# Performance work log

Hardware: AMD Instinct MI355X
Metric: run time of the kernel (lower is better)

Reference implementation:

```python
import jax, jax.numpy as jnp
import numpy as np

N = 100000
E = 3200000
C = 32

def setup_inputs() -> dict:
    key = jax.random.key(0)
    k1, k2, k3, k4 = jax.random.split(key, 4)
    adj = jax.random.uniform(k1, (E,), dtype=jnp.float32)          # per-edge weights
    labels = jax.random.uniform(k2, (N, C), dtype=jnp.float32)     # node label distributions
    src = jax.random.randint(k3, (E,), 0, N, dtype=jnp.int64)
    dst = jax.random.randint(k4, (E,), 0, N, dtype=jnp.int64)
    return {"adj": adj, "labels": labels, "src": src, "dst": dst, "n_lpa": 3}

def reference(adj, labels, src, dst, n_lpa):
    # One hop of label propagation: msg_e = label[src_e] * w_e; out_v = sum_{e: dst_e=v} msg_e
    n_nodes = labels.shape[0]

    def lp(lab):
        msg = lab[src] * adj[:, None]                 # [E, C] gather-multiply
        return jax.ops.segment_sum(msg, dst, num_segments=n_nodes)  # scatter-sum over dst

    # soft_label == 0 path of the original forward: plain iterated propagation
    for _ in range(n_lpa):
        labels = lp(labels)
    return labels
```

## Files before the change

### kernel.cpp

```cpp
#include <hip/hip_runtime.h>
#include <hip/hip_bf16.h>


#define LPA_C   32
#define BKT_LG  7
#define BKT_NV  (1 << BKT_LG)
#define CHUNK   12800

__global__ __launch_bounds__(1024)
void k_histA(const int* __restrict__ dst, int* __restrict__ C,
             int E, int P, int nbkt) {
    __shared__ int h[1024];
    int c = blockIdx.x;
    int base = c * CHUNK;
    int lim = min(CHUNK, E - base);
    for (int i = threadIdx.x; i < nbkt; i += 1024) h[i] = 0;
    __syncthreads();
    for (int i = threadIdx.x; i < lim; i += 1024)
        atomicAdd(&h[dst[base + i] >> BKT_LG], 1);
    __syncthreads();
    for (int i = threadIdx.x; i < nbkt; i += 1024) C[i * P + c] = h[i];
}

__global__ void k_scanC(int* __restrict__ C, int* __restrict__ btot, int P) {
    __shared__ int s[256];
    int b = blockIdx.x;
    int t = threadIdx.x;
    int v = (t < P) ? C[b * P + t] : 0;
    s[t] = v;
    __syncthreads();
    for (int off = 1; off < 256; off <<= 1) {
        int x = (t >= off) ? s[t - off] : 0;
        __syncthreads();
        s[t] += x;
        __syncthreads();
    }
    if (t < P) C[b * P + t] = s[t] - v;
    if (t == 255) btot[b] = s[255];
}

__global__ __launch_bounds__(1024)
void k_scanB(const int* __restrict__ btot, int* __restrict__ bstart,
             int* __restrict__ row_start, int nb, int N, int E) {
    __shared__ int s[1024];
    int t = threadIdx.x;
    int v = (t < nb) ? btot[t] : 0;
    s[t] = v;
    __syncthreads();
    for (int off = 1; off < 1024; off <<= 1) {
        int x = (t >= off) ? s[t - off] : 0;
        __syncthreads();
        s[t] += x;
        __syncthreads();
    }
    if (t < nb) bstart[t] = s[t] - v;
    if (t == 0) { bstart[nb] = E; row_start[N] = E; }
}

__global__ __launch_bounds__(1024)
void k_scatA(const int* __restrict__ src, const int* __restrict__ dst,
             const float* __restrict__ adj, const int* __restrict__ C,
             const int* __restrict__ bstart, int2* __restrict__ mid,
             int E, int P, int nbkt) {
    __shared__ int cur[1024];
    int c = blockIdx.x;
    int base = c * CHUNK;
    int lim = min(CHUNK, E - base);
    for (int i = threadIdx.x; i < nbkt; i += 1024)
        cur[i] = bstart[i] + C[i * P + c];
    __syncthreads();
    for (int i = threadIdx.x; i < lim; i += 1024) {
        int d = dst[base + i];
        int b = d >> BKT_LG;
        int pos = atomicAdd(&cur[b], 1);
        mid[pos] = make_int2(src[base + i] | ((d & (BKT_NV - 1)) << 20),
                             __float_as_int(adj[base + i]));
    }
}

__global__ __launch_bounds__(512)
void k_sortnode(const int2* __restrict__ mid, const int* __restrict__ bstart,
                int2* __restrict__ edges, int* __restrict__ row_start, int N) {
    __shared__ int lcnt[BKT_NV];
    __shared__ int lofs[BKT_NV];
    int b = blockIdx.x;
    int s0 = bstart[b], e0 = bstart[b + 1];
    int v0 = b << BKT_LG;
    int nv = min(BKT_NV, N - v0);

    if (threadIdx.x < BKT_NV) lcnt[threadIdx.x] = 0;
    __syncthreads();
    for (int i = s0 + threadIdx.x; i < e0; i += 512)
        atomicAdd(&lcnt[mid[i].x >> 20], 1);
    __syncthreads();
    if (threadIdx.x < BKT_NV) lofs[threadIdx.x] = lcnt[threadIdx.x];
    __syncthreads();
    for (int off = 1; off < BKT_NV; off <<= 1) {
        int x = 0;
        if (threadIdx.x < BKT_NV && threadIdx.x >= off) x = lofs[threadIdx.x - off];
        __syncthreads();
        if (threadIdx.x < BKT_NV) lofs[threadIdx.x] += x;
        __syncthreads();
    }
    if (threadIdx.x < BKT_NV) {
        int base = s0 + lofs[threadIdx.x] - lcnt[threadIdx.x];
        lcnt[threadIdx.x] = base;
        if (threadIdx.x < nv) row_start[v0 + threadIdx.x] = base;
    }
    __syncthreads();
    for (int i = s0 + threadIdx.x; i < e0; i += 512) {
        int2 ed = mid[i];
        int pos = atomicAdd(&lcnt[ed.x >> 20], 1);
        edges[pos] = make_int2(ed.x & 0xFFFFF, ed.y);
    }
}

__global__ void k_tobf16(const float* __restrict__ in, ushort* __restrict__ out, int n) {
    int i = blockIdx.x * blockDim.x + threadIdx.x;
    if (i < n) out[i] = __bfloat16_as_ushort(__float2bfloat16(in[i]));
}

template <int OUT16>
__global__ void lpa_pull16(const int2* __restrict__ edges,
                           const int* __restrict__ row_start,
                           const ushort* __restrict__ lab_in,
                           void* __restrict__ out_v, int N) {
    int node = blockIdx.x * 8 + (threadIdx.x >> 5);
    int c = threadIdx.x & 31;
    if (node >= N) return;
    int j = row_start[node];
    int end = row_start[node + 1];
    float acc0 = 0.f, acc1 = 0.f;
#define GATH(S) (__uint_as_float((unsigned)lab_in[((size_t)(unsigned)(S) << 5) + c] << 16))
    for (; j + 8 <= end; j += 8) {
        int4 q0 = *(const int4*)(edges + j);
        int4 q1 = *(const int4*)(edges + j + 2);
        int4 q2 = *(const int4*)(edges + j + 4);
        int4 q3 = *(const int4*)(edges + j + 6);
        acc0 += __int_as_float(q0.y) * GATH(q0.x);
        acc1 += __int_as_float(q0.w) * GATH(q0.z);
        acc0 += __int_as_float(q1.y) * GATH(q1.x);
        acc1 += __int_as_float(q1.w) * GATH(q1.z);
        acc0 += __int_as_float(q2.y) * GATH(q2.x);
        acc1 += __int_as_float(q2.w) * GATH(q2.z);
        acc0 += __int_as_float(q3.y) * GATH(q3.x);
        acc1 += __int_as_float(q3.w) * GATH(q3.z);
    }
    for (; j < end; ++j) {
        int2 e = edges[j];
        acc0 += __int_as_float(e.y) * GATH(e.x);
    }
#undef GATH
    float acc = acc0 + acc1;
    if (OUT16) {
        ((ushort*)out_v)[((size_t)node << 5) + c] =
            __bfloat16_as_ushort(__float2bfloat16(acc));
    } else {
        ((float*)out_v)[((size_t)node << 5) + c] = acc;
    }
}

__global__ void lpa_scatter_fb(const float* __restrict__ adj,
                               const float* __restrict__ lab_in,
                               const int* __restrict__ src,
                               const int* __restrict__ dst,
                               float* __restrict__ out, int E) {
    long long idx = (long long)blockIdx.x * blockDim.x + threadIdx.x;
    int e = (int)(idx >> 5);
    if (e >= E) return;
    int c = (int)(idx & 31);
    float v = lab_in[(long long)src[e] * LPA_C + c] * adj[e];
    unsafeAtomicAdd(&out[(long long)dst[e] * LPA_C + c], v);
}

extern "C" void kernel_launch(void* const* d_in, const int* in_sizes, int n_in,
                              void* d_out, int out_size, void* d_ws, size_t ws_size,
                              hipStream_t stream) {
    const float* adj    = (const float*)d_in[0];
    const float* labels = (const float*)d_in[1];
    const int*   src    = (const int*)d_in[2];
    const int*   dst    = (const int*)d_in[3];

    const int E  = in_sizes[0];
    const int NC = in_sizes[1];
    const int N  = NC / LPA_C;
    const int NBKT = (N + BKT_NV - 1) >> BKT_LG;
    const int P  = (E + CHUNK - 1) / CHUNK;
    float* out = (float*)d_out;

    char* p = (char*)d_ws;
    int2*  edges     = (int2*)p;  p += (size_t)E * sizeof(int2);
    int2*  mid       = (int2*)p;  p += (size_t)E * sizeof(int2);
    int*   C         = (int*)p;   p += (size_t)NBKT * P * sizeof(int);
    int*   btot      = (int*)p;   p += (size_t)NBKT * sizeof(int);
    int*   bstart    = (int*)p;   p += (size_t)(NBKT + 1) * sizeof(int);
    int*   row_start = (int*)p;   p += (size_t)(N + 1) * sizeof(int);
    size_t needed = (size_t)(p - (char*)d_ws);
    ushort* lab16_a = (ushort*)mid;
    ushort* lab16_b = (ushort*)mid + (size_t)NC;

    if (ws_size < needed || NBKT > 1024 || P > 256 || N >= (1 << 20)) {
        float* ws0 = (float*)d_ws;
        const size_t nbytes = (size_t)NC * sizeof(float);
        const long long total = (long long)E * LPA_C;
        const unsigned grid = (unsigned)((total + 255) / 256);
        hipMemsetAsync(out, 0, nbytes, stream);
        lpa_scatter_fb<<<grid, 256, 0, stream>>>(adj, labels, src, dst, out, E);
        hipMemsetAsync(ws0, 0, nbytes, stream);
        lpa_scatter_fb<<<grid, 256, 0, stream>>>(adj, out, src, dst, ws0, E);
        hipMemsetAsync(out, 0, nbytes, stream);
        lpa_scatter_fb<<<grid, 256, 0, stream>>>(adj, ws0, src, dst, out, E);
        return;
    }

    k_histA   <<<P, 1024, 0, stream>>>(dst, C, E, P, NBKT);
    k_scanC   <<<NBKT, 256, 0, stream>>>(C, btot, P);
    k_scanB   <<<1, 1024, 0, stream>>>(btot, bstart, row_start, NBKT, N, E);
    k_scatA   <<<P, 1024, 0, stream>>>(src, dst, adj, C, bstart, mid, E, P, NBKT);
    k_sortnode<<<NBKT, 512, 0, stream>>>(mid, bstart, edges, row_start, N);

    k_tobf16<<<(NC + 255) / 256, 256, 0, stream>>>(labels, lab16_a, NC);

    const unsigned gridN = (unsigned)((N + 7) / 8);
    lpa_pull16<1><<<gridN, 256, 0, stream>>>(edges, row_start, lab16_a, lab16_b, N);
    lpa_pull16<1><<<gridN, 256, 0, stream>>>(edges, row_start, lab16_b, lab16_a, N);
    lpa_pull16<0><<<gridN, 256, 0, stream>>>(edges, row_start, lab16_a, out, N);
}
```

Measured before the change: 252.0 us.

## Stage bucket scatter in shared memory for coalesced global writes

The bucket-scatter kernel now sorts each chunk's edges locally in LDS: it recomputes a per-chunk bucket histogram, scans it, and places edges into a shared buffer. It then writes them out to their global bucket positions in contiguous runs, using a binary search to find each element's bucket. Chunk size is halved and block size drops to 512 so the 6400-entry int2 staging array fits in LDS, and the per-bucket scan is widened to handle up to 512 partitions. The aim is to replace scattered 8-byte global writes with mostly coalesced ones. The cost is a redundant histogram pass, an in-block scan, a per-element binary search and more blocks.

```diff
diff --git a/kernel.cpp b/kernel.cpp
--- a/kernel.cpp
+++ b/kernel.cpp
@@ -5,38 +5,39 @@
 #define LPA_C   32
 #define BKT_LG  7
 #define BKT_NV  (1 << BKT_LG)
-#define CHUNK   12800
-
-__global__ __launch_bounds__(1024)
+#define CHUNK   6400
+
+__global__ __launch_bounds__(512)
 void k_histA(const int* __restrict__ dst, int* __restrict__ C,
              int E, int P, int nbkt) {
     __shared__ int h[1024];
     int c = blockIdx.x;
     int base = c * CHUNK;
     int lim = min(CHUNK, E - base);
-    for (int i = threadIdx.x; i < nbkt; i += 1024) h[i] = 0;
-    __syncthreads();
-    for (int i = threadIdx.x; i < lim; i += 1024)
+    for (int i = threadIdx.x; i < nbkt; i += 512) h[i] = 0;
+    __syncthreads();
+    for (int i = threadIdx.x; i < lim; i += 512)
         atomicAdd(&h[dst[base + i] >> BKT_LG], 1);
     __syncthreads();
-    for (int i = threadIdx.x; i < nbkt; i += 1024) C[i * P + c] = h[i];
-}
-
-__global__ void k_scanC(int* __restrict__ C, int* __restrict__ btot, int P) {
-    __shared__ int s[256];
+    for (int i = threadIdx.x; i < nbkt; i += 512) C[i * P + c] = h[i];
+}
+
+__global__ __launch_bounds__(512)
+void k_scanC(int* __restrict__ C, int* __restrict__ btot, int P) {
+    __shared__ int s[512];
     int b = blockIdx.x;
     int t = threadIdx.x;
     int v = (t < P) ? C[b * P + t] : 0;
     s[t] = v;
     __syncthreads();
-    for (int off = 1; off < 256; off <<= 1) {
+    for (int off = 1; off < 512; off <<= 1) {
         int x = (t >= off) ? s[t - off] : 0;
         __syncthreads();
         s[t] += x;
         __syncthreads();
     }
     if (t < P) C[b * P + t] = s[t] - v;
-    if (t == 255) btot[b] = s[255];
+    if (t == 511) btot[b] = s[511];
 }
 
 __global__ __launch_bounds__(1024)
@@ -57,24 +58,63 @@
     if (t == 0) { bstart[nb] = E; row_start[N] = E; }
 }
 
-__global__ __launch_bounds__(1024)
+__global__ __launch_bounds__(512)
 void k_scatA(const int* __restrict__ src, const int* __restrict__ dst,
              const float* __restrict__ adj, const int* __restrict__ C,
              const int* __restrict__ bstart, int2* __restrict__ mid,
              int E, int P, int nbkt) {
-    __shared__ int cur[1024];
+    __shared__ int2 sedge[CHUNK];
+    __shared__ int  lofs[1025];
+    __shared__ int  cur[1024];
+    __shared__ int  s2[512];
     int c = blockIdx.x;
     int base = c * CHUNK;
     int lim = min(CHUNK, E - base);
-    for (int i = threadIdx.x; i < nbkt; i += 1024)
-        cur[i] = bstart[i] + C[i * P + c];
-    __syncthreads();
-    for (int i = threadIdx.x; i < lim; i += 1024) {
+    int t = threadIdx.x;
+
+    for (int i = t; i < nbkt; i += 512) cur[i] = 0;
+    __syncthreads();
+    for (int i = t; i < lim; i += 512)
+        atomicAdd(&cur[dst[base + i] >> BKT_LG], 1);
+    __syncthreads();
+
+    int k0 = 2 * t, k1 = 2 * t + 1;
+    int a0 = (k0 < nbkt) ? cur[k0] : 0;
+    int a1 = (k1 < nbkt) ? cur[k1] : 0;
+    int ts = a0 + a1;
+    s2[t] = ts;
+    __syncthreads();
+    for (int off = 1; off < 512; off <<= 1) {
+        int x = (t >= off) ? s2[t - off] : 0;
+        __syncthreads();
+        s2[t] += x;
+        __syncthreads();
+    }
+    int pre = s2[t] - ts;
+    if (k0 < nbkt) lofs[k0] = pre;
+    if (k1 < nbkt) lofs[k1] = pre + a0;
+    if (t == 0) lofs[nbkt] = lim;
+    __syncthreads();
+    for (int i = t; i < nbkt; i += 512) cur[i] = lofs[i];
+    __syncthreads();
+
+    for (int i = t; i < lim; i += 512) {
         int d = dst[base + i];
         int b = d >> BKT_LG;
         int pos = atomicAdd(&cur[b], 1);
-        mid[pos] = make_int2(src[base + i] | ((d & (BKT_NV - 1)) << 20),
-                             __float_as_int(adj[base + i]));
+        sedge[pos] = make_int2(src[base + i] | ((d & (BKT_NV - 1)) << 20),
+                               __float_as_int(adj[base + i]));
+    }
+    __syncthreads();
+
+    for (int i = t; i < lim; i += 512) {
+        int lo = 0, hi = nbkt;
+        while (hi - lo > 1) {
+            int m = (lo + hi) >> 1;
+            if (lofs[m] <= i) lo = m; else hi = m;
+        }
+        int gdst = bstart[lo] + C[lo * P + c] + (i - lofs[lo]);
+        mid[gdst] = sedge[i];
     }
 }
 
@@ -199,7 +239,7 @@
     ushort* lab16_a = (ushort*)mid;
     ushort* lab16_b = (ushort*)mid + (size_t)NC;
 
-    if (ws_size < needed || NBKT > 1024 || P > 256 || N >= (1 << 20)) {
+    if (ws_size < needed || NBKT > 1024 || P > 512 || N >= (1 << 20)) {
         float* ws0 = (float*)d_ws;
         const size_t nbytes = (size_t)NC * sizeof(float);
         const long long total = (long long)E * LPA_C;
@@ -213,10 +253,10 @@
         return;
     }
 
-    k_histA   <<<P, 1024, 0, stream>>>(dst, C, E, P, NBKT);
-    k_scanC   <<<NBKT, 256, 0, stream>>>(C, btot, P);
+    k_histA   <<<P, 512, 0, stream>>>(dst, C, E, P, NBKT);
+    k_scanC   <<<NBKT, 512, 0, stream>>>(C, btot, P);
     k_scanB   <<<1, 1024, 0, stream>>>(btot, bstart, row_start, NBKT, N, E);
-    k_scatA   <<<P, 1024, 0, stream>>>(src, dst, adj, C, bstart, mid, E, P, NBKT);
+    k_scatA   <<<P, 512, 0, stream>>>(src, dst, adj, C, bstart, mid, E, P, NBKT);
     k_sortnode<<<NBKT, 512, 0, stream>>>(mid, bstart, edges, row_start, N);
 
     k_tobf16<<<(NC + 255) / 256, 256, 0, stream>>>(labels, lab16_a, NC);
```

Result: no change. 251.0 us (-0.4%).
